# Performance work log

Measured on AMD Instinct MI355X. Metric: run time of the kernel, lower is better.

## Reference

```python
import jax, jax.numpy as jnp
import numpy as np

D_MODEL = 1024
N_HEADS = 16
D_K = D_MODEL // N_HEADS
B, S = 4, 2048
NEG = -1e9


def setup_inputs() -> dict:
    key = jax.random.key(0)
    ks = jax.random.split(key, 9)
    scale = 1.0 / np.sqrt(D_MODEL)
    x = jax.random.normal(ks[0], (B, S, D_MODEL), dtype=jnp.float32)
    mask = jnp.tril(jnp.ones((S, S), dtype=jnp.int32))  # causal lower-triangular
    Wq = jax.random.normal(ks[1], (D_MODEL, D_MODEL), dtype=jnp.float32) * scale
    Wk = jax.random.normal(ks[2], (D_MODEL, D_MODEL), dtype=jnp.float32) * scale
    Wv = jax.random.normal(ks[3], (D_MODEL, D_MODEL), dtype=jnp.float32) * scale
    Wo = jax.random.normal(ks[4], (D_MODEL, D_MODEL), dtype=jnp.float32) * scale
    bq = jnp.zeros((D_MODEL,), dtype=jnp.float32)
    bk = jnp.zeros((D_MODEL,), dtype=jnp.float32)
    bv = jnp.zeros((D_MODEL,), dtype=jnp.float32)
    bo = jnp.zeros((D_MODEL,), dtype=jnp.float32)
    return {"x": x, "mask": mask, "Wq": Wq, "bq": bq, "Wk": Wk, "bk": bk,
            "Wv": Wv, "bv": bv, "Wo": Wo, "bo": bo}


def reference(x, mask, Wq, bq, Wk, bk, Wv, bv, Wo, bo):
    b, s, _ = x.shape
    # nn.Linear: y = x @ W.T + b
    Q = x @ Wq.T + bq
    K = x @ Wk.T + bk
    V = x @ Wv.T + bv
    # [b, h, s, d_k]
    Q = Q.reshape(b, s, N_HEADS, D_K).transpose(0, 2, 1, 3)
    K = K.reshape(b, s, N_HEADS, D_K).transpose(0, 2, 1, 3)
    V = V.reshape(b, s, N_HEADS, D_K).transpose(0, 2, 1, 3)
    score = jnp.einsum('bhqd,bhkd->bhqk', Q, K) / jnp.sqrt(jnp.float32(D_K))
    score = jnp.where(mask == 0, jnp.float32(NEG), score)
    attn = jax.nn.softmax(score, axis=-1)
    out = jnp.einsum('bhqk,bhkd->bhqd', attn, V)
    out = out.transpose(0, 2, 1, 3).reshape(b, s, D_MODEL)
    return out @ Wo.T + bo
```

## Files before the change

### kernel.cpp

```cpp
#include <hip/hip_runtime.h>
#include <hip/hip_bf16.h>
#include <stdint.h>

typedef __bf16 bf16x8 __attribute__((ext_vector_type(8)));
typedef float  f32x4  __attribute__((ext_vector_type(4)));

#define B_   4
#define S_   2048
#define DM   1024
#define H_   16
#define DK   64
#define M_TOT 8192

__device__ __forceinline__ void gld16(const __bf16* g, char* l) {
    __builtin_amdgcn_global_load_lds(
        (const __attribute__((address_space(1))) void*)g,
        (__attribute__((address_space(3))) void*)l,
        16, 0, 0);
}

__global__ __launch_bounds__(256)
void cvt_all(const float* __restrict__ x,
             const float* __restrict__ w0, const float* __restrict__ w1,
             const float* __restrict__ w2, const float* __restrict__ w3,
             __bf16* __restrict__ xb, __bf16* __restrict__ wb) {
    int i = (blockIdx.x * 256 + threadIdx.x) * 8;
    const float* in;
    __bf16* out;
    if (i < M_TOT * DM) {
        in = x + i; out = xb + i;
    } else {
        int j = i - M_TOT * DM;
        int w = j >> 20;
        const float* ws4[4] = {w0, w1, w2, w3};
        in = ws4[w] + (j & 1048575); out = wb + j;
    }
    float4 a = *(const float4*)in;
    float4 c = *(const float4*)(in + 4);
    bf16x8 o;
    o[0] = (__bf16)a.x; o[1] = (__bf16)a.y; o[2] = (__bf16)a.z; o[3] = (__bf16)a.w;
    o[4] = (__bf16)c.x; o[5] = (__bf16)c.y; o[6] = (__bf16)c.z; o[7] = (__bf16)c.w;
    *(bf16x8*)out = o;
}

__device__ __forceinline__ void gemm_core(const __bf16* __restrict__ A,
                                          const __bf16* __restrict__ W,
                                          int m0, int n0,
                                          f32x4 (&acc)[4][4]) {
    __shared__ __bf16 As[128 * 64];
    __shared__ __bf16 Bs[128 * 64];
    const int tid  = threadIdx.x;
    const int wid  = tid >> 6;
    const int lane = tid & 63;
    const int ln15 = lane & 15, lg = lane >> 4;
    const int wr = (wid >> 1) * 64;
    const int wc = (wid & 1) * 64;

    const int r0 = tid >> 3;
    const int sc = ((tid & 7) ^ (r0 & 7)) * 8;
    uint32_t aoff[4], boff[4];
#pragma unroll
    for (int i = 0; i < 4; ++i) {
        aoff[i] = (uint32_t)((m0 + r0 + i * 32) * DM + sc);
        boff[i] = (uint32_t)((n0 + r0 + i * 32) * DM + sc);
    }
    char* la = (char*)As + wid * 1024;
    char* lb = (char*)Bs + wid * 1024;
    const int rsw = ln15 & 7;

    for (int k0 = 0; k0 < DM; k0 += 64) {
        const __bf16* Ak = A + k0;
        const __bf16* Wk = W + k0;
#pragma unroll
        for (int i = 0; i < 4; ++i) {
            gld16(Ak + aoff[i], la + i * 4096);
            gld16(Wk + boff[i], lb + i * 4096);
        }
        __syncthreads();
#pragma unroll
        for (int kk = 0; kk < 2; ++kk) {
            bf16x8 af[4], bfr[4];
#pragma unroll
            for (int m = 0; m < 4; ++m)
                af[m] = *(const bf16x8*)&As[(wr + m * 16 + ln15) * 64 + (((kk * 4 + lg) ^ rsw) * 8)];
#pragma unroll
            for (int n = 0; n < 4; ++n)
                bfr[n] = *(const bf16x8*)&Bs[(wc + n * 16 + ln15) * 64 + (((kk * 4 + lg) ^ rsw) * 8)];
#pragma unroll
            for (int m = 0; m < 4; ++m)
#pragma unroll
                for (int n = 0; n < 4; ++n)
                    acc[m][n] = __builtin_amdgcn_mfma_f32_16x16x32_bf16(af[m], bfr[n], acc[m][n], 0, 0, 0);
        }
        __syncthreads();
    }
}

__global__ __launch_bounds__(256)
void gemm_qkv_kernel(const __bf16* __restrict__ Xb,
                     const __bf16* __restrict__ Wq, const __bf16* __restrict__ Wk,
                     const __bf16* __restrict__ Wv,
                     const float* __restrict__ bq, const float* __restrict__ bk,
                     const float* __restrict__ bv,
                     __bf16* __restrict__ Qb, __bf16* __restrict__ Kb,
                     __bf16* __restrict__ Vt) {
    const int z = blockIdx.z;
    const __bf16* W   = (z == 0) ? Wq : (z == 1) ? Wk : Wv;
    const float* bias = (z == 0) ? bq : (z == 1) ? bk : bv;
    const int m0 = blockIdx.x * 128, n0 = blockIdx.y * 128;

    f32x4 acc[4][4] = {};
    gemm_core(Xb, W, m0, n0, acc);

    const int tid = threadIdx.x, wid = tid >> 6, lane = tid & 63;
    const int ln15 = lane & 15, lg = lane >> 4;
    const int wr = (wid >> 1) * 64, wc = (wid & 1) * 64;
    const float oscl = (z == 0) ? 0.18033688f : 1.0f;

    if (z < 2) {
        __bf16* out = (z == 0) ? Qb : Kb;
#pragma unroll
        for (int ni = 0; ni < 4; ++ni) {
            int col = n0 + wc + ni * 16 + ln15;
            int h = col >> 6, d = col & 63;
            float bval = bias[col];
#pragma unroll
            for (int mi = 0; mi < 4; ++mi)
#pragma unroll
                for (int r = 0; r < 4; ++r) {
                    int row = m0 + wr + mi * 16 + lg * 4 + r;
                    int b = row >> 11, s = row & 2047;
                    out[(((size_t)(b * H_ + h)) * S_ + s) * DK + d] =
                        (__bf16)((acc[mi][ni][r] + bval) * oscl);
                }
        }
    } else {
#pragma unroll
        for (int ni = 0; ni < 4; ++ni) {
            int col = n0 + wc + ni * 16 + ln15;
            int h = col >> 6, d = col & 63;
            float bval = bias[col];
#pragma unroll
            for (int mi = 0; mi < 4; ++mi)
#pragma unroll
                for (int r = 0; r < 4; ++r) {
                    int row = m0 + wr + mi * 16 + lg * 4 + r;
                    int b = row >> 11, s = row & 2047;
                    Vt[(((size_t)(b * H_ + h)) * DK + d) * S_ + s] =
                        (__bf16)(acc[mi][ni][r] + bval);
                }
        }
    }
}

__global__ __launch_bounds__(256)
void gemm_out_kernel(const __bf16* __restrict__ Ab, const __bf16* __restrict__ Wo,
                     const float* __restrict__ bo, float* __restrict__ out) {
    const int m0 = blockIdx.x * 128, n0 = blockIdx.y * 128;
    f32x4 acc[4][4] = {};
    gemm_core(Ab, Wo, m0, n0, acc);

    const int tid = threadIdx.x, wid = tid >> 6, lane = tid & 63;
    const int ln15 = lane & 15, lg = lane >> 4;
    const int wr = (wid >> 1) * 64, wc = (wid & 1) * 64;
#pragma unroll
    for (int ni = 0; ni < 4; ++ni) {
        int col = n0 + wc + ni * 16 + ln15;
        float bval = bo[col];
#pragma unroll
        for (int mi = 0; mi < 4; ++mi)
#pragma unroll
            for (int r = 0; r < 4; ++r) {
                int row = m0 + wr + mi * 16 + lg * 4 + r;
                out[(size_t)row * DM + col] = acc[mi][ni][r] + bval;
            }
    }
}

__global__ __launch_bounds__(512)
void attn_kernel(const __bf16* __restrict__ Qb, const __bf16* __restrict__ Kb,
                 const __bf16* __restrict__ Vt, __bf16* __restrict__ AO) {
    __shared__ __bf16 Ks[2][128 * 64];
    __shared__ __bf16 Vs[2][64 * 128];

    const int tid = threadIdx.x, wid = tid >> 6, lane = tid & 63;
    const int ln15 = lane & 15, lg = lane >> 4;
    const int bh = blockIdx.x;
    const int p  = blockIdx.y;
    const size_t base = (size_t)bh * (S_ * DK);
    const int b = bh >> 4, h = bh & 15;

    const int krow = wid * 8 + (lane >> 3);
    const int kswz = ((lane & 7) ^ (krow & 7)) * 8;
    const int vrow = wid * 4 + (lane >> 4);
    const int vswz = ((lane & 15) ^ (vrow & 15)) * 8;
    const int swz  = (ln15 & 7) << 3;

    const uint32_t ko1 = (uint32_t)(krow * DK + kswz);
    const uint32_t ko2 = (uint32_t)((krow + 64) * DK + kswz);
    const uint32_t vo1 = (uint32_t)(vrow * S_ + vswz);
    const uint32_t vo2 = (uint32_t)((vrow + 32) * S_ + vswz);

    const __bf16* kgb = Kb + base;
    const __bf16* vgb = Vt + base;

    auto stage = [&](int buf, int kt) {
        char* dk = (char*)Ks + buf * 16384 + wid * 1024;
        char* dv = (char*)Vs + buf * 16384 + wid * 1024;
        const __bf16* kk_ = kgb + kt * (128 * DK);
        const __bf16* vv_ = vgb + kt * 128;
        gld16(kk_ + ko1, dk);
        gld16(kk_ + ko2, dk + 8192);
        gld16(vv_ + vo1, dv);
        gld16(vv_ + vo2, dv + 8192);
    };

    bf16x8 ones;
#pragma unroll
    for (int j = 0; j < 8; ++j) ones[j] = (__bf16)1.0f;

#pragma unroll
    for (int ph = 0; ph < 2; ++ph) {
        const int qb   = ph ? p : 15 - p;
        const int last = qb;
        const int qr0  = qb * 128 + wid * 16 + ln15;

        bf16x8 qf[2];
        {
            int q0 = qr0;
            qf[0] = *(const bf16x8*)&Qb[base + (size_t)q0 * DK + lg * 8];
            qf[1] = *(const bf16x8*)&Qb[base + (size_t)q0 * DK + 32 + lg * 8];
        }

        f32x4 acc[4] = {};
        f32x4 lacc = {};

        __builtin_amdgcn_s_barrier();
        stage(0, 0);
        asm volatile("s_waitcnt vmcnt(0)" ::: "memory");
        __builtin_amdgcn_s_barrier();
        __builtin_amdgcn_sched_barrier(0);

        for (int kt = 0; kt <= last; ++kt) {
            const int cur = kt & 1;
            if (kt < last) stage(cur ^ 1, kt + 1);

            const __bf16* ksb = &Ks[cur][0];
            const __bf16* vsb = &Vs[cur][0];

            f32x4 z[8] = {};
            __builtin_amdgcn_s_setprio(1);
#pragma unroll
            for (int cb = 0; cb < 8; ++cb)
#pragma unroll
                for (int kk = 0; kk < 2; ++kk) {
                    bf16x8 kf = *(const bf16x8*)&ksb[(cb * 16 + ln15) * 64 + ((kk * 32 + lg * 8) ^ swz)];
                    z[cb] = __builtin_amdgcn_mfma_f32_16x16x32_bf16(kf, qf[kk], z[cb], 0, 0, 0);
                }
            __builtin_amdgcn_s_setprio(0);

            if (kt == last) {
                const int kcb = kt * 128 + lg * 4;
#pragma unroll
                for (int cb = 0; cb < 8; ++cb)
#pragma unroll
                    for (int r = 0; r < 4; ++r)
                        if (kcb + cb * 16 + r > qr0) z[cb][r] = -3e8f;
            }

            uint32_t a0[8], b0[8];
#pragma unroll
            for (int cb = 0; cb < 8; ++cb) {
                float e0 = exp2f(z[cb][0]), e1 = exp2f(z[cb][1]);
                float e2 = exp2f(z[cb][2]), e3 = exp2f(z[cb][3]);
                asm("v_cvt_pk_bf16_f32 %0, %1, %2" : "=v"(a0[cb]) : "v"(e0), "v"(e1));
                asm("v_cvt_pk_bf16_f32 %0, %1, %2" : "=v"(b0[cb]) : "v"(e2), "v"(e3));
            }

            union U8 { uint32_t u[4]; bf16x8 v; };
            bf16x8 pa[4];
#pragma unroll
            for (int ks = 0; ks < 4; ++ks) {
                uint32_t x = a0[2 * ks], y = a0[2 * ks + 1];
                asm("v_permlane32_swap_b32 %0, %1" : "+v"(x), "+v"(y));
                asm("v_permlane16_swap_b32 %0, %1" : "+v"(x), "+v"(y));
                uint32_t p2 = b0[2 * ks], q2 = b0[2 * ks + 1];
                asm("v_permlane32_swap_b32 %0, %1" : "+v"(p2), "+v"(q2));
                asm("v_permlane16_swap_b32 %0, %1" : "+v"(p2), "+v"(q2));
                U8 f; f.u[0] = x; f.u[1] = p2; f.u[2] = y; f.u[3] = q2;
                pa[ks] = f.v;
            }

            __builtin_amdgcn_s_setprio(1);
#pragma unroll
            for (int ks = 0; ks < 4; ++ks) {
                lacc = __builtin_amdgcn_mfma_f32_16x16x32_bf16(pa[ks], ones, lacc, 0, 0, 0);
#pragma unroll
                for (int db = 0; db < 4; ++db) {
                    bf16x8 vf = *(const bf16x8*)&vsb[(db * 16 + ln15) * 128 + (((ks * 4 + lg) ^ ln15) * 8)];
                    acc[db] = __builtin_amdgcn_mfma_f32_16x16x32_bf16(pa[ks], vf, acc[db], 0, 0, 0);
                }
            }
            __builtin_amdgcn_s_setprio(0);

            if (kt < last) {
                asm volatile("s_waitcnt vmcnt(0)" ::: "memory");
                __builtin_amdgcn_s_barrier();
                __builtin_amdgcn_sched_barrier(0);
            }
        }

#pragma unroll
        for (int r = 0; r < 4; ++r) {
            float i0 = 1.f / lacc[r];
            int s0r = qb * 128 + wid * 16 + lg * 4 + r;
#pragma unroll
            for (int db = 0; db < 4; ++db)
                AO[((size_t)(b * S_ + s0r)) * DM + h * DK + db * 16 + ln15] = (__bf16)(acc[db][r] * i0);
        }
    }
}

extern "C" void kernel_launch(void* const* d_in, const int* in_sizes, int n_in,
                              void* d_out, int out_size, void* d_ws, size_t ws_size,
                              hipStream_t stream) {
    const float* x  = (const float*)d_in[0];
    const float* Wq = (const float*)d_in[2];
    const float* bq = (const float*)d_in[3];
    const float* Wk = (const float*)d_in[4];
    const float* bk = (const float*)d_in[5];
    const float* Wv = (const float*)d_in[6];
    const float* bv = (const float*)d_in[7];
    const float* Wo = (const float*)d_in[8];
    const float* bo = (const float*)d_in[9];
    float* out = (float*)d_out;

    char* ws = (char*)d_ws;
    __bf16* xb  = (__bf16*)ws;
    __bf16* wqb = (__bf16*)(ws + 16777216);
    __bf16* wkb = wqb + 1048576;
    __bf16* wvb = wkb + 1048576;
    __bf16* wob = wvb + 1048576;
    __bf16* Qb  = (__bf16*)(ws + 25165824);
    __bf16* Kb  = Qb + 8388608;
    __bf16* Vt  = Kb + 8388608;
    __bf16* AO  = xb;

    cvt_all<<<6144, 256, 0, stream>>>(x, Wq, Wk, Wv, Wo, xb, wqb);

    gemm_qkv_kernel<<<dim3(64, 8, 3), 256, 0, stream>>>(xb, wqb, wkb, wvb,
                                                        bq, bk, bv, Qb, Kb, Vt);
    attn_kernel<<<dim3(64, 8), 512, 0, stream>>>(Qb, Kb, Vt, AO);
    gemm_out_kernel<<<dim3(64, 8), 256, 0, stream>>>(AO, wob, bo, out);
}
```

Measured before the change: 168.1 us.

## Double-buffer GEMM LDS tiles with K=32 stages to overlap loads and MFMA

The shared GEMM core changes from a single 64-wide K tile, loaded and then computed between two __syncthreads, to two 32-wide K buffers. The next tile's async global-to-LDS loads are issued before the current tile's MFMAs, so memory latency is meant to hide behind compute, and one barrier per step replaces two. The LDS swizzle is reworked for the 32-column layout. In exchange the steps get smaller: 32 iterations with 16 MFMAs each, and a full vmcnt(0) wait every step, which may limit how much latency is actually hidden.

```diff
diff --git a/kernel.cpp b/kernel.cpp
--- a/kernel.cpp
+++ b/kernel.cpp
@@ -47,8 +47,8 @@
                                           const __bf16* __restrict__ W,
                                           int m0, int n0,
                                           f32x4 (&acc)[4][4]) {
-    __shared__ __bf16 As[128 * 64];
-    __shared__ __bf16 Bs[128 * 64];
+    __shared__ __bf16 As[2][128 * 32];
+    __shared__ __bf16 Bs[2][128 * 32];
     const int tid  = threadIdx.x;
     const int wid  = tid >> 6;
     const int lane = tid & 63;
@@ -56,43 +56,57 @@
     const int wr = (wid >> 1) * 64;
     const int wc = (wid & 1) * 64;
 
-    const int r0 = tid >> 3;
-    const int sc = ((tid & 7) ^ (r0 & 7)) * 8;
-    uint32_t aoff[4], boff[4];
-#pragma unroll
-    for (int i = 0; i < 4; ++i) {
-        aoff[i] = (uint32_t)((m0 + r0 + i * 32) * DM + sc);
-        boff[i] = (uint32_t)((n0 + r0 + i * 32) * DM + sc);
-    }
-    char* la = (char*)As + wid * 1024;
-    char* lb = (char*)Bs + wid * 1024;
-    const int rsw = ln15 & 7;
-
-    for (int k0 = 0; k0 < DM; k0 += 64) {
+    const int c1 = tid, c2 = tid + 256;
+    const int sc1 = (((c1 & 3) ^ ((c1 >> 3) & 3))) * 8;
+    const int sc2 = (((c2 & 3) ^ ((c2 >> 3) & 3))) * 8;
+    const uint32_t ao1 = (uint32_t)((m0 + (c1 >> 2)) * DM + sc1);
+    const uint32_t ao2 = (uint32_t)((m0 + (c2 >> 2)) * DM + sc2);
+    const uint32_t bo1 = (uint32_t)((n0 + (c1 >> 2)) * DM + sc1);
+    const uint32_t bo2 = (uint32_t)((n0 + (c2 >> 2)) * DM + sc2);
+    char* la0 = (char*)&As[0][0] + wid * 1024;
+    char* lb0 = (char*)&Bs[0][0] + wid * 1024;
+    const int rsw = ((ln15 >> 1) & 3);
+
+    auto stage = [&](int buf, int k0) {
+        char* la = la0 + buf * 8192;
+        char* lb = lb0 + buf * 8192;
         const __bf16* Ak = A + k0;
         const __bf16* Wk = W + k0;
-#pragma unroll
-        for (int i = 0; i < 4; ++i) {
-            gld16(Ak + aoff[i], la + i * 4096);
-            gld16(Wk + boff[i], lb + i * 4096);
-        }
-        __syncthreads();
-#pragma unroll
-        for (int kk = 0; kk < 2; ++kk) {
-            bf16x8 af[4], bfr[4];
-#pragma unroll
-            for (int m = 0; m < 4; ++m)
-                af[m] = *(const bf16x8*)&As[(wr + m * 16 + ln15) * 64 + (((kk * 4 + lg) ^ rsw) * 8)];
+        gld16(Ak + ao1, la);
+        gld16(Ak + ao2, la + 4096);
+        gld16(Wk + bo1, lb);
+        gld16(Wk + bo2, lb + 4096);
+    };
+
+    stage(0, 0);
+    asm volatile("s_waitcnt vmcnt(0)" ::: "memory");
+    __builtin_amdgcn_s_barrier();
+    __builtin_amdgcn_sched_barrier(0);
+
+    for (int t = 0; t < 32; ++t) {
+        const int cur = t & 1;
+        if (t < 31) stage(cur ^ 1, (t + 1) * 32);
+
+        const __bf16* as = &As[cur][0];
+        const __bf16* bs = &Bs[cur][0];
+        bf16x8 af[4], bfr[4];
+#pragma unroll
+        for (int m = 0; m < 4; ++m)
+            af[m] = *(const bf16x8*)&as[(wr + m * 16 + ln15) * 32 + ((lg ^ rsw) * 8)];
+#pragma unroll
+        for (int n = 0; n < 4; ++n)
+            bfr[n] = *(const bf16x8*)&bs[(wc + n * 16 + ln15) * 32 + ((lg ^ rsw) * 8)];
+#pragma unroll
+        for (int m = 0; m < 4; ++m)
 #pragma unroll
             for (int n = 0; n < 4; ++n)
-                bfr[n] = *(const bf16x8*)&Bs[(wc + n * 16 + ln15) * 64 + (((kk * 4 + lg) ^ rsw) * 8)];
-#pragma unroll
-            for (int m = 0; m < 4; ++m)
-#pragma unroll
-                for (int n = 0; n < 4; ++n)
-                    acc[m][n] = __builtin_amdgcn_mfma_f32_16x16x32_bf16(af[m], bfr[n], acc[m][n], 0, 0, 0);
-        }
-        __syncthreads();
+                acc[m][n] = __builtin_amdgcn_mfma_f32_16x16x32_bf16(af[m], bfr[n], acc[m][n], 0, 0, 0);
+
+        if (t < 31) {
+            asm volatile("s_waitcnt vmcnt(0)" ::: "memory");
+            __builtin_amdgcn_s_barrier();
+            __builtin_amdgcn_sched_barrier(0);
+        }
     }
 }
 
```

Measured after the change: 190.1 us. 13.1% more time.
